# Kernel optimization log

Hardware: AMD Instinct MI355X
Metric: run time of the kernel (lower is better)

The kernel has to match this reference:

```python
import jax, jax.numpy as jnp
import numpy as np

HEADS = 8
DIM_HEAD = 64
SCALE = DIM_HEAD ** -0.5

def setup_inputs() -> dict:
    key = jax.random.key(0)
    ks = jax.random.split(key, 6)
    b, n, m, qd, cd = 4, 2048, 2048, 256, 256
    inner = HEADS * DIM_HEAD
    return {
        "x": jax.random.normal(ks[0], (b, n, qd), jnp.float32),
        "context": jax.random.normal(ks[1], (b, m, cd), jnp.float32),
        "Wq": jax.random.normal(ks[2], (inner, qd), jnp.float32) * 0.02,
        "bq": jnp.zeros((inner,), jnp.float32),
        "Wkv": jax.random.normal(ks[3], (2 * inner, cd), jnp.float32) * 0.02,
        "bkv": jnp.zeros((2 * inner,), jnp.float32),
        "Wo": jax.random.normal(ks[4], (qd, inner), jnp.float32) * 0.02,
        "bo": jnp.zeros((qd,), jnp.float32),
    }

def reference(x, context, Wq, bq, Wkv, bkv, Wo, bo):
    b, n, _ = x.shape
    m = context.shape[1]
    inner = HEADS * DIM_HEAD
    # 1x1 conv projections == pointwise linear
    q = jnp.einsum('bnd,ed->bne', x, Wq) + bq            # [b, n, inner]
    kv = jnp.einsum('bmd,ed->bme', context, Wkv) + bkv    # [b, m, 2*inner]
    k, v = kv[..., :inner], kv[..., inner:]
    q = q.reshape(b, n, HEADS, DIM_HEAD).transpose(0, 2, 1, 3)  # [b,h,n,d]
    k = k.reshape(b, m, HEADS, DIM_HEAD).transpose(0, 2, 1, 3)
    v = v.reshape(b, m, HEADS, DIM_HEAD).transpose(0, 2, 1, 3)
    sim = jnp.einsum('bhid,bhjd->bhij', q, k) * SCALE     # [b,h,n,m]
    attn = jax.nn.softmax(sim, axis=-1)
    out = jnp.einsum('bhij,bhjd->bhid', attn, v)          # [b,h,n,d]
    out = out.transpose(0, 2, 1, 3).reshape(b, n, inner)  # [b,n,inner]
    return jnp.einsum('bne,oe->bno', out, Wo) + bo        # [b,n,query_dim]
```

## Files before the change

kernel.cpp:

```cpp
#include <hip/hip_runtime.h>
#include <hip/hip_bf16.h>

#define NB 4
#define SEQ 2048
#define NHEADS 8
#define ROWS (NB * SEQ)

typedef __attribute__((ext_vector_type(8))) short bf16x8;
typedef __attribute__((ext_vector_type(4))) short bf16x4;
typedef __attribute__((ext_vector_type(4))) float f32x4;
typedef __attribute__((ext_vector_type(16))) float f32x16;

__device__ inline short f2bf(float x) {
    union { float f; unsigned u; } v; v.f = x;
    unsigned r = v.u + 0x7FFF + ((v.u >> 16) & 1);
    return (short)(r >> 16);
}

__device__ inline unsigned pack2bf(float a, float b) {
    __hip_bfloat162 h = __float22bfloat162_rn(make_float2(a, b));
    unsigned u; __builtin_memcpy(&u, &h, 4);
    return u;
}

__device__ inline unsigned comb2(unsigned w1, unsigned w2, float inv) {
    union { unsigned v; float f; } a, b, c, d;
    a.v = w1 << 16;          b.v = w2 << 16;
    c.v = w1 & 0xffff0000u;  d.v = w2 & 0xffff0000u;
    return pack2bf((a.f + b.f) * inv, (c.f + d.f) * inv);
}

__global__ __launch_bounds__(256) void cvt_all(
    const float* __restrict__ x, const float* __restrict__ ctx,
    const float* __restrict__ wq, const float* __restrict__ wkv,
    const float* __restrict__ wo,
    short* __restrict__ xb, short* __restrict__ cb, short* __restrict__ wqb,
    short* __restrict__ wkvb, short* __restrict__ wob)
{
    const int i = blockIdx.x * 256 + threadIdx.x;
    const float* src; short* dst; int off;
    if (i < 524288)       { src = x;   dst = xb;   off = i; }
    else if (i < 1048576) { src = ctx; dst = cb;   off = i - 524288; }
    else if (i < 1081344) { src = wq;  dst = wqb;  off = i - 1048576; }
    else if (i < 1146880) { src = wkv; dst = wkvb; off = i - 1081344; }
    else                  { src = wo;  dst = wob;  off = i - 1146880; }
    const float4 v = ((const float4*)src)[off];
    uint2 o2;
    o2.x = pack2bf(v.x, v.y);
    o2.y = pack2bf(v.z, v.w);
    *(uint2*)(dst + (size_t)off * 4) = o2;
}

__global__ __launch_bounds__(256, 3) void proj2(
    const short* __restrict__ xb, const short* __restrict__ wqb,
    const float* __restrict__ bq,
    const short* __restrict__ cb, const short* __restrict__ wkvb,
    const float* __restrict__ bkv,
    short* __restrict__ q2b, short* __restrict__ kv2b, float qscale)
{
    __shared__ short As[128 * 64];
    __shared__ short Ws[128 * 64];
    const int tid = threadIdx.x;
    const int bid = blockIdx.x;
    const int w = tid >> 6, lane = tid & 63, low = lane & 15, quad = lane >> 4;
    const int wm = w >> 1, wn = w & 1;
    const int K = 256;

    const short* A; const short* W; const float* bias;
    short* outp; int Ccols; float scale; int rM0, c0;
    if (bid < 512) {
        A = cb; W = wkvb; bias = bkv; outp = kv2b; Ccols = 1024; scale = 1.0f;
        c0 = (bid & 7) * 128; rM0 = (bid >> 3) * 128;
    } else {
        const int u = bid - 512;
        A = xb; W = wqb; bias = bq; outp = q2b; Ccols = 512; scale = qscale;
        c0 = (u & 3) * 128; rM0 = (u >> 2) * 128;
    }

    const int srow = tid >> 3, sj = tid & 7;

    f32x4 acc[4][4];
#pragma unroll
    for (int mt = 0; mt < 4; ++mt)
#pragma unroll
        for (int nt = 0; nt < 4; ++nt) acc[mt][nt] = (f32x4){0.f, 0.f, 0.f, 0.f};

    bf16x8 pab[4], pwb[4];
#pragma unroll
    for (int c = 0; c < 4; ++c) {
        const int row = c * 32 + srow;
        pab[c] = *(const bf16x8*)(A + (size_t)(rM0 + row) * K + sj * 8);
        pwb[c] = *(const bf16x8*)(W + (size_t)(c0 + row) * K + sj * 8);
    }

    int k0 = 0;
    for (;;) {
        __syncthreads();
#pragma unroll
        for (int c = 0; c < 4; ++c) {
            const int row = c * 32 + srow;
            const int pc = sj ^ (row & 7);
            *(bf16x8*)(&As[row * 64 + pc * 8]) = pab[c];
            *(bf16x8*)(&Ws[row * 64 + pc * 8]) = pwb[c];
        }
        __syncthreads();
        const int kn = k0 + 64;
        if (kn < K) {
#pragma unroll
            for (int c = 0; c < 4; ++c) {
                const int row = c * 32 + srow;
                pab[c] = *(const bf16x8*)(A + (size_t)(rM0 + row) * K + kn + sj * 8);
                pwb[c] = *(const bf16x8*)(W + (size_t)(c0 + row) * K + kn + sj * 8);
            }
        }
#pragma unroll
        for (int kh = 0; kh < 2; ++kh) {
            bf16x8 af[4], bfv[4];
#pragma unroll
            for (int t = 0; t < 4; ++t) {
                const int ra = wm * 64 + t * 16 + low;
                af[t] = *(const bf16x8*)(&As[ra * 64 + ((kh * 4 + quad) ^ (ra & 7)) * 8]);
                const int rb = wn * 64 + t * 16 + low;
                bfv[t] = *(const bf16x8*)(&Ws[rb * 64 + ((kh * 4 + quad) ^ (rb & 7)) * 8]);
            }
#pragma unroll
            for (int mt = 0; mt < 4; ++mt)
#pragma unroll
                for (int nt = 0; nt < 4; ++nt)
                    acc[mt][nt] = __builtin_amdgcn_mfma_f32_16x16x32_bf16(af[mt], bfv[nt], acc[mt][nt], 0, 0, 0);
        }
        k0 = kn;
        if (k0 >= K) break;
    }

#pragma unroll
    for (int nt = 0; nt < 4; ++nt) {
        const int col = c0 + wn * 64 + nt * 16 + low;
        const float bv = bias[col];
#pragma unroll
        for (int mt = 0; mt < 4; ++mt) {
            const size_t rbase = (size_t)(rM0 + wm * 64 + mt * 16 + quad * 4);
#pragma unroll
            for (int r = 0; r < 4; ++r)
                outp[(rbase + r) * Ccols + col] = f2bf((acc[mt][nt][r] + bv) * scale);
        }
    }
}

__global__ __launch_bounds__(256, 2) void gemm64_ocomb(
    const short* __restrict__ num, const float* __restrict__ lbuf,
    const short* __restrict__ W, const float* __restrict__ bias,
    float* __restrict__ out)
{
    const int K = 512, Ccols = 256;
    const size_t NHALF = (size_t)ROWS * 512;
    const int R8 = ROWS * 8;
    __shared__ short As[2][64 * 64];
    __shared__ short Ws[2][64 * 64];
    const int tid = threadIdx.x;
    const int w = tid >> 6, lane = tid & 63, low = lane & 15, quad = lane >> 4;
    const int wm = w >> 1, wn = w & 1;

    const int d = blockIdx.x;
    const int c8 = d & 7, j = d >> 3;
    const int xcol = j & 3;
    const int y = ((j >> 2) << 3) + c8;
    const int r0 = y * 64, c0 = xcol * 64;

    const int srow = tid >> 2;
    const int sc = (tid & 3) * 2;

    f32x4 acc[2][2];
#pragma unroll
    for (int mt = 0; mt < 2; ++mt)
#pragma unroll
        for (int nt = 0; nt < 2; ++nt) acc[mt][nt] = (f32x4){0.f, 0.f, 0.f, 0.f};

    uint4 pa1[2], pa2[2];
    float pinv;
    bf16x8 pwb[2];

    auto loadA = [&](int k0) {
        const int hh = k0 >> 6;
        const int row = r0 + srow;
        pinv = lbuf[row * 8 + hh] + lbuf[R8 + row * 8 + hh];
        const short* p1 = num + (size_t)row * 512 + k0 + sc * 8;
        pa1[0] = ((const uint4*)p1)[0];
        pa1[1] = ((const uint4*)p1)[1];
        const short* p2 = p1 + NHALF;
        pa2[0] = ((const uint4*)p2)[0];
        pa2[1] = ((const uint4*)p2)[1];
    };
    auto loadW = [&](int k0) {
        const short* p = W + (size_t)(c0 + srow) * K + k0 + sc * 8;
        pwb[0] = ((const bf16x8*)p)[0];
        pwb[1] = ((const bf16x8*)p)[1];
    };
    auto stage = [&](int bi) {
        const float inv = 1.f / pinv;
#pragma unroll
        for (int c = 0; c < 2; ++c) {
            const int pc = (sc + c) ^ (srow & 7);
            union { unsigned u[4]; bf16x8 v; } r;
            r.u[0] = comb2(pa1[c].x, pa2[c].x, inv);
            r.u[1] = comb2(pa1[c].y, pa2[c].y, inv);
            r.u[2] = comb2(pa1[c].z, pa2[c].z, inv);
            r.u[3] = comb2(pa1[c].w, pa2[c].w, inv);
            *(bf16x8*)(&As[bi][srow * 64 + pc * 8]) = r.v;
            *(bf16x8*)(&Ws[bi][srow * 64 + pc * 8]) = pwb[c];
        }
    };

    loadA(0); loadW(0);
    stage(0);
    __syncthreads();

    const int NT = K / 64;
    for (int t = 0; t < NT; ++t) {
        if (t + 1 < NT) { loadA((t + 1) * 64); loadW((t + 1) * 64); }

        const short* Ac = &As[t & 1][0];
        const short* Wc = &Ws[t & 1][0];
#pragma unroll
        for (int kh = 0; kh < 2; ++kh) {
            bf16x8 af[2], bfv[2];
#pragma unroll
            for (int tt = 0; tt < 2; ++tt) {
                const int ra = wm * 32 + tt * 16 + low;
                af[tt] = *(const bf16x8*)(&Ac[ra * 64 + ((kh * 4 + quad) ^ (ra & 7)) * 8]);
                const int rb = wn * 32 + tt * 16 + low;
                bfv[tt] = *(const bf16x8*)(&Wc[rb * 64 + ((kh * 4 + quad) ^ (rb & 7)) * 8]);
            }
#pragma unroll
            for (int mt = 0; mt < 2; ++mt)
#pragma unroll
                for (int nt = 0; nt < 2; ++nt)
                    acc[mt][nt] = __builtin_amdgcn_mfma_f32_16x16x32_bf16(af[mt], bfv[nt], acc[mt][nt], 0, 0, 0);
        }

        if (t + 1 < NT) stage((t + 1) & 1);
        __syncthreads();
    }

#pragma unroll
    for (int nt = 0; nt < 2; ++nt) {
        const int col = c0 + wn * 32 + nt * 16 + low;
        const float bv = bias[col];
#pragma unroll
        for (int mt = 0; mt < 2; ++mt) {
            const size_t rbase = (size_t)(r0 + wm * 32 + mt * 16 + quad * 4);
#pragma unroll
            for (int r = 0; r < 4; ++r)
                out[(rbase + r) * Ccols + col] = acc[mt][nt][r] + bv;
        }
    }
}

#define KST 72
#define VST 72

__global__ __launch_bounds__(256, 4) void attn_mfma(
    const short* __restrict__ q2,
    const short* __restrict__ kv2,
    short* __restrict__ numb,
    float* __restrict__ lbuf)
{
    __shared__ short Ks[64 * KST];
    __shared__ short Vt[64 * VST];

    const int tid = threadIdx.x;
    const int w = tid >> 6;
    const int lane = tid & 63;
    const int l31 = lane & 31;
    const int h2 = lane >> 5;

    const int flat = blockIdx.x;
    const int h = flat & 7;
    const int rest = flat >> 3;
    const int half = rest & 1;
    const int rest2 = rest >> 1;
    const int qtile = rest2 & 15;
    const int b = rest2 >> 4;
    const int iq0 = qtile * 128;
    const int jt0 = half * 16;

    bf16x8 qr[4];
#pragma unroll
    for (int st = 0; st < 4; ++st)
        qr[st] = *(const bf16x8*)(q2 + (size_t)(b * SEQ + iq0 + w * 32 + l31) * 512
                                  + h * 64 + st * 16 + h2 * 8);

    const short* kbase = kv2 + (size_t)(b * SEQ) * 1024 + h * 64;
    const short* vbase = kbase + 512;

    float lsum = 0.f;
    f32x16 oacc[2];
#pragma unroll
    for (int dg = 0; dg < 2; ++dg)
#pragma unroll
        for (int r = 0; r < 16; ++r) oacc[dg][r] = 0.f;

    const int krow = tid >> 2;
    const int kc = (tid & 3) * 16;
    const int vk4 = (tid & 15) * 4;
    const int vd4 = (tid >> 4) * 4;

    bf16x8 pk0, pk1;
    bf16x4 pv0, pv1, pv2, pv3;
    {
        const short* ksrc = kbase + (size_t)(jt0 * 64 + krow) * 1024 + kc;
        pk0 = *(const bf16x8*)(ksrc);
        pk1 = *(const bf16x8*)(ksrc + 8);
        const short* vs = vbase + (size_t)(jt0 * 64 + vk4) * 1024 + vd4;
        pv0 = *(const bf16x4*)(vs);
        pv1 = *(const bf16x4*)(vs + 1024);
        pv2 = *(const bf16x4*)(vs + 2048);
        pv3 = *(const bf16x4*)(vs + 3072);
    }

    for (int jt = jt0; jt < jt0 + 16; ++jt) {
        __syncthreads();
        *(bf16x8*)(&Ks[krow * KST + kc]) = pk0;
        *(bf16x8*)(&Ks[krow * KST + kc + 8]) = pk1;
        {
            bf16x4 c0_, c1_, c2_, c3_;
            c0_[0] = pv0[0]; c0_[1] = pv1[0]; c0_[2] = pv2[0]; c0_[3] = pv3[0];
            c1_[0] = pv0[1]; c1_[1] = pv1[1]; c1_[2] = pv2[1]; c1_[3] = pv3[1];
            c2_[0] = pv0[2]; c2_[1] = pv1[2]; c2_[2] = pv2[2]; c2_[3] = pv3[2];
            c3_[0] = pv0[3]; c3_[1] = pv1[3]; c3_[2] = pv2[3]; c3_[3] = pv3[3];
            *(bf16x4*)(&Vt[(vd4 + 0) * VST + vk4]) = c0_;
            *(bf16x4*)(&Vt[(vd4 + 1) * VST + vk4]) = c1_;
            *(bf16x4*)(&Vt[(vd4 + 2) * VST + vk4]) = c2_;
            *(bf16x4*)(&Vt[(vd4 + 3) * VST + vk4]) = c3_;
        }
        __syncthreads();

        if (jt + 1 < jt0 + 16) {
            const short* ksrc = kbase + (size_t)((jt + 1) * 64 + krow) * 1024 + kc;
            pk0 = *(const bf16x8*)(ksrc);
            pk1 = *(const bf16x8*)(ksrc + 8);
            const short* vs = vbase + (size_t)((jt + 1) * 64 + vk4) * 1024 + vd4;
            pv0 = *(const bf16x4*)(vs);
            pv1 = *(const bf16x4*)(vs + 1024);
            pv2 = *(const bf16x4*)(vs + 2048);
            pv3 = *(const bf16x4*)(vs + 3072);
        }

        bf16x8 pfrag[4];
#pragma unroll
        for (int kg = 0; kg < 2; ++kg) {
            f32x16 s;
#pragma unroll
            for (int r = 0; r < 16; ++r) s[r] = 0.f;
#pragma unroll
            for (int st = 0; st < 4; ++st) {
                const bf16x8 kf = *(const bf16x8*)(&Ks[(kg * 32 + l31) * KST + st * 16 + h2 * 8]);
                s = __builtin_amdgcn_mfma_f32_32x32x16_bf16(kf, qr[st], s, 0, 0, 0);
            }
            unsigned wv[8];
#pragma unroll
            for (int g = 0; g < 4; ++g) {
                const float p0 = __builtin_amdgcn_exp2f(s[4 * g + 0]);
                const float p1 = __builtin_amdgcn_exp2f(s[4 * g + 1]);
                const float p2 = __builtin_amdgcn_exp2f(s[4 * g + 2]);
                const float p3 = __builtin_amdgcn_exp2f(s[4 * g + 3]);
                lsum += (p0 + p1) + (p2 + p3);
                wv[2 * g]     = pack2bf(p0, p1);
                wv[2 * g + 1] = pack2bf(p2, p3);
            }
#pragma unroll
            for (int q = 0; q < 2; ++q) {
                unsigned a0 = wv[4 * q + 0], b0 = wv[4 * q + 2];
                unsigned a1 = wv[4 * q + 1], b1 = wv[4 * q + 3];
                asm volatile("v_permlane32_swap_b32 %0, %1" : "+v"(a0), "+v"(b0));
                asm volatile("v_permlane32_swap_b32 %0, %1" : "+v"(a1), "+v"(b1));
                union { unsigned u[4]; bf16x8 v; } f;
                f.u[0] = a0; f.u[1] = a1; f.u[2] = b0; f.u[3] = b1;
                pfrag[kg * 2 + q] = f.v;
            }
        }

#pragma unroll
        for (int st = 0; st < 4; ++st) {
            const bf16x8 pf = pfrag[st];
#pragma unroll
            for (int dg = 0; dg < 2; ++dg) {
                const bf16x8 vf = *(const bf16x8*)(&Vt[(dg * 32 + l31) * VST + st * 16 + h2 * 8]);
                oacc[dg] = __builtin_amdgcn_mfma_f32_32x32x16_bf16(pf, vf, oacc[dg], 0, 0, 0);
            }
        }
    }

    lsum += __shfl_xor(lsum, 32);
    short* nb = numb + (size_t)half * ROWS * 512;
    float* lb = lbuf + (size_t)half * ROWS * 8;
    if (lane < 32)
        lb[(size_t)(b * SEQ + iq0 + w * 32 + l31) * 8 + h] = lsum;
#pragma unroll
    for (int dg = 0; dg < 2; ++dg)
#pragma unroll
        for (int r = 0; r < 16; ++r) {
            const int qrow = w * 32 + (r & 3) + 8 * (r >> 2) + 4 * h2;
            nb[(size_t)(b * SEQ + iq0 + qrow) * 512 + h * 64 + dg * 32 + l31] =
                f2bf(oacc[dg][r]);
        }
}

extern "C" void kernel_launch(void* const* d_in, const int* in_sizes, int n_in,
                              void* d_out, int out_size, void* d_ws, size_t ws_size,
                              hipStream_t stream) {
    const float* x   = (const float*)d_in[0];
    const float* ctx = (const float*)d_in[1];
    const float* Wq  = (const float*)d_in[2];
    const float* bq  = (const float*)d_in[3];
    const float* Wkv = (const float*)d_in[4];
    const float* bkv = (const float*)d_in[5];
    const float* Wo  = (const float*)d_in[6];
    const float* bo  = (const float*)d_in[7];
    float* out = (float*)d_out;

    short* xb   = (short*)d_ws;
    short* cb   = xb + (size_t)ROWS * 256;
    short* wqb  = cb + (size_t)ROWS * 256;
    short* wkvb = wqb + 131072;
    short* wob  = wkvb + 262144;
    short* q2b  = wob + 131072;
    short* kv2b = q2b + (size_t)ROWS * 512;
    short* numb = kv2b + (size_t)ROWS * 1024;
    float* lbuf = (float*)(numb + (size_t)2 * ROWS * 512);

    const float qscale = 0.125f * 1.44269504088896f;

    cvt_all<<<4608, 256, 0, stream>>>(x, ctx, Wq, Wkv, Wo,
                                      xb, cb, wqb, wkvb, wob);
    proj2<<<768, 256, 0, stream>>>(xb, wqb, bq, cb, wkvb, bkv,
                                   q2b, kv2b, qscale);
    attn_mfma<<<NB * NHEADS * (SEQ / 128) * 2, 256, 0, stream>>>(
        q2b, kv2b, numb, lbuf);
    gemm64_ocomb<<<512, 256, 0, stream>>>(numb, lbuf, wob, bo, out);
}
```

Measured before the change: 152.5 us.

## Move split-K attention combine into the block via LDS reduction

Previously each attention block handled 128 queries over half the keys and wrote partial bf16 numerators plus row sums, which the output GEMM then combined and normalized. Now each block handles 64 queries. The four warps split into two query groups and two key halves, double-buffered in LDS, and the halves are reduced through shared memory so a normalized output is written directly. This removes the double-sized partial buffer traffic and the combine arithmetic in the output GEMM. In exchange it uses twice the LDS, cuts the occupancy hint from 4 to 2, and adds an in-block reduction step.

```diff
diff --git a/kernel.cpp b/kernel.cpp
--- a/kernel.cpp
+++ b/kernel.cpp
@@ -21,13 +21,6 @@
     __hip_bfloat162 h = __float22bfloat162_rn(make_float2(a, b));
     unsigned u; __builtin_memcpy(&u, &h, 4);
     return u;
-}
-
-__device__ inline unsigned comb2(unsigned w1, unsigned w2, float inv) {
-    union { unsigned v; float f; } a, b, c, d;
-    a.v = w1 << 16;          b.v = w2 << 16;
-    c.v = w1 & 0xffff0000u;  d.v = w2 & 0xffff0000u;
-    return pack2bf((a.f + b.f) * inv, (c.f + d.f) * inv);
 }
 
 __global__ __launch_bounds__(256) void cvt_all(
@@ -147,14 +140,11 @@
     }
 }
 
-__global__ __launch_bounds__(256, 2) void gemm64_ocomb(
-    const short* __restrict__ num, const float* __restrict__ lbuf,
-    const short* __restrict__ W, const float* __restrict__ bias,
-    float* __restrict__ out)
+__global__ __launch_bounds__(256, 2) void gemm64_o(
+    const short* __restrict__ Ab, const short* __restrict__ W,
+    const float* __restrict__ bias, float* __restrict__ out)
 {
     const int K = 512, Ccols = 256;
-    const size_t NHALF = (size_t)ROWS * 512;
-    const int R8 = ROWS * 8;
     __shared__ short As[2][64 * 64];
     __shared__ short Ws[2][64 * 64];
     const int tid = threadIdx.x;
@@ -176,20 +166,12 @@
 #pragma unroll
         for (int nt = 0; nt < 2; ++nt) acc[mt][nt] = (f32x4){0.f, 0.f, 0.f, 0.f};
 
-    uint4 pa1[2], pa2[2];
-    float pinv;
-    bf16x8 pwb[2];
+    bf16x8 pa[2], pwb[2];
 
     auto loadA = [&](int k0) {
-        const int hh = k0 >> 6;
-        const int row = r0 + srow;
-        pinv = lbuf[row * 8 + hh] + lbuf[R8 + row * 8 + hh];
-        const short* p1 = num + (size_t)row * 512 + k0 + sc * 8;
-        pa1[0] = ((const uint4*)p1)[0];
-        pa1[1] = ((const uint4*)p1)[1];
-        const short* p2 = p1 + NHALF;
-        pa2[0] = ((const uint4*)p2)[0];
-        pa2[1] = ((const uint4*)p2)[1];
+        const short* p = Ab + (size_t)(r0 + srow) * 512 + k0 + sc * 8;
+        pa[0] = ((const bf16x8*)p)[0];
+        pa[1] = ((const bf16x8*)p)[1];
     };
     auto loadW = [&](int k0) {
         const short* p = W + (size_t)(c0 + srow) * K + k0 + sc * 8;
@@ -197,16 +179,10 @@
         pwb[1] = ((const bf16x8*)p)[1];
     };
     auto stage = [&](int bi) {
-        const float inv = 1.f / pinv;
 #pragma unroll
         for (int c = 0; c < 2; ++c) {
             const int pc = (sc + c) ^ (srow & 7);
-            union { unsigned u[4]; bf16x8 v; } r;
-            r.u[0] = comb2(pa1[c].x, pa2[c].x, inv);
-            r.u[1] = comb2(pa1[c].y, pa2[c].y, inv);
-            r.u[2] = comb2(pa1[c].z, pa2[c].z, inv);
-            r.u[3] = comb2(pa1[c].w, pa2[c].w, inv);
-            *(bf16x8*)(&As[bi][srow * 64 + pc * 8]) = r.v;
+            *(bf16x8*)(&As[bi][srow * 64 + pc * 8]) = pa[c];
             *(bf16x8*)(&Ws[bi][srow * 64 + pc * 8]) = pwb[c];
         }
     };
@@ -259,35 +235,33 @@
 #define KST 72
 #define VST 72
 
-__global__ __launch_bounds__(256, 4) void attn_mfma(
+__global__ __launch_bounds__(256, 2) void attn_mfma(
     const short* __restrict__ q2,
     const short* __restrict__ kv2,
-    short* __restrict__ numb,
-    float* __restrict__ lbuf)
+    short* __restrict__ ob)
 {
-    __shared__ short Ks[64 * KST];
-    __shared__ short Vt[64 * VST];
+    __shared__ short Ks[2][64 * KST];
+    __shared__ short Vt[2][64 * VST];
 
     const int tid = threadIdx.x;
     const int w = tid >> 6;
     const int lane = tid & 63;
     const int l31 = lane & 31;
     const int h2 = lane >> 5;
+    const int wq = w & 1;
+    const int wh = w >> 1;
 
     const int flat = blockIdx.x;
     const int h = flat & 7;
     const int rest = flat >> 3;
-    const int half = rest & 1;
-    const int rest2 = rest >> 1;
-    const int qtile = rest2 & 15;
-    const int b = rest2 >> 4;
-    const int iq0 = qtile * 128;
-    const int jt0 = half * 16;
+    const int qtile = rest & 31;
+    const int b = rest >> 5;
+    const int iq0 = qtile * 64;
 
     bf16x8 qr[4];
 #pragma unroll
     for (int st = 0; st < 4; ++st)
-        qr[st] = *(const bf16x8*)(q2 + (size_t)(b * SEQ + iq0 + w * 32 + l31) * 512
+        qr[st] = *(const bf16x8*)(q2 + (size_t)(b * SEQ + iq0 + wq * 32 + l31) * 512
                                   + h * 64 + st * 16 + h2 * 8);
 
     const short* kbase = kv2 + (size_t)(b * SEQ) * 1024 + h * 64;
@@ -305,47 +279,56 @@
     const int vk4 = (tid & 15) * 4;
     const int vd4 = (tid >> 4) * 4;
 
-    bf16x8 pk0, pk1;
-    bf16x4 pv0, pv1, pv2, pv3;
-    {
-        const short* ksrc = kbase + (size_t)(jt0 * 64 + krow) * 1024 + kc;
-        pk0 = *(const bf16x8*)(ksrc);
-        pk1 = *(const bf16x8*)(ksrc + 8);
-        const short* vs = vbase + (size_t)(jt0 * 64 + vk4) * 1024 + vd4;
-        pv0 = *(const bf16x4*)(vs);
-        pv1 = *(const bf16x4*)(vs + 1024);
-        pv2 = *(const bf16x4*)(vs + 2048);
-        pv3 = *(const bf16x4*)(vs + 3072);
-    }
-
-    for (int jt = jt0; jt < jt0 + 16; ++jt) {
+    bf16x8 pk0[2], pk1[2];
+    bf16x4 pv0[2], pv1[2], pv2[2], pv3[2];
+#pragma unroll
+    for (int t = 0; t < 2; ++t) {
+        const int kt = t * 16;
+        const short* ksrc = kbase + (size_t)(kt * 64 + krow) * 1024 + kc;
+        pk0[t] = *(const bf16x8*)(ksrc);
+        pk1[t] = *(const bf16x8*)(ksrc + 8);
+        const short* vs = vbase + (size_t)(kt * 64 + vk4) * 1024 + vd4;
+        pv0[t] = *(const bf16x4*)(vs);
+        pv1[t] = *(const bf16x4*)(vs + 1024);
+        pv2[t] = *(const bf16x4*)(vs + 2048);
+        pv3[t] = *(const bf16x4*)(vs + 3072);
+    }
+
+    for (int jt = 0; jt < 16; ++jt) {
         __syncthreads();
-        *(bf16x8*)(&Ks[krow * KST + kc]) = pk0;
-        *(bf16x8*)(&Ks[krow * KST + kc + 8]) = pk1;
-        {
+#pragma unroll
+        for (int t = 0; t < 2; ++t) {
+            *(bf16x8*)(&Ks[t][krow * KST + kc]) = pk0[t];
+            *(bf16x8*)(&Ks[t][krow * KST + kc + 8]) = pk1[t];
             bf16x4 c0_, c1_, c2_, c3_;
-            c0_[0] = pv0[0]; c0_[1] = pv1[0]; c0_[2] = pv2[0]; c0_[3] = pv3[0];
-            c1_[0] = pv0[1]; c1_[1] = pv1[1]; c1_[2] = pv2[1]; c1_[3] = pv3[1];
-            c2_[0] = pv0[2]; c2_[1] = pv1[2]; c2_[2] = pv2[2]; c2_[3] = pv3[2];
-            c3_[0] = pv0[3]; c3_[1] = pv1[3]; c3_[2] = pv2[3]; c3_[3] = pv3[3];
-            *(bf16x4*)(&Vt[(vd4 + 0) * VST + vk4]) = c0_;
-            *(bf16x4*)(&Vt[(vd4 + 1) * VST + vk4]) = c1_;
-            *(bf16x4*)(&Vt[(vd4 + 2) * VST + vk4]) = c2_;
-            *(bf16x4*)(&Vt[(vd4 + 3) * VST + vk4]) = c3_;
+            c0_[0] = pv0[t][0]; c0_[1] = pv1[t][0]; c0_[2] = pv2[t][0]; c0_[3] = pv3[t][0];
+            c1_[0] = pv0[t][1]; c1_[1] = pv1[t][1]; c1_[2] = pv2[t][1]; c1_[3] = pv3[t][1];
+            c2_[0] = pv0[t][2]; c2_[1] = pv1[t][2]; c2_[2] = pv2[t][2]; c2_[3] = pv3[t][2];
+            c3_[0] = pv0[t][3]; c3_[1] = pv1[t][3]; c3_[2] = pv2[t][3]; c3_[3] = pv3[t][3];
+            *(bf16x4*)(&Vt[t][(vd4 + 0) * VST + vk4]) = c0_;
+            *(bf16x4*)(&Vt[t][(vd4 + 1) * VST + vk4]) = c1_;
+            *(bf16x4*)(&Vt[t][(vd4 + 2) * VST + vk4]) = c2_;
+            *(bf16x4*)(&Vt[t][(vd4 + 3) * VST + vk4]) = c3_;
         }
         __syncthreads();
 
-        if (jt + 1 < jt0 + 16) {
-            const short* ksrc = kbase + (size_t)((jt + 1) * 64 + krow) * 1024 + kc;
-            pk0 = *(const bf16x8*)(ksrc);
-            pk1 = *(const bf16x8*)(ksrc + 8);
-            const short* vs = vbase + (size_t)((jt + 1) * 64 + vk4) * 1024 + vd4;
-            pv0 = *(const bf16x4*)(vs);
-            pv1 = *(const bf16x4*)(vs + 1024);
-            pv2 = *(const bf16x4*)(vs + 2048);
-            pv3 = *(const bf16x4*)(vs + 3072);
-        }
-
+        if (jt + 1 < 16) {
+#pragma unroll
+            for (int t = 0; t < 2; ++t) {
+                const int kt = t * 16 + jt + 1;
+                const short* ksrc = kbase + (size_t)(kt * 64 + krow) * 1024 + kc;
+                pk0[t] = *(const bf16x8*)(ksrc);
+                pk1[t] = *(const bf16x8*)(ksrc + 8);
+                const short* vs = vbase + (size_t)(kt * 64 + vk4) * 1024 + vd4;
+                pv0[t] = *(const bf16x4*)(vs);
+                pv1[t] = *(const bf16x4*)(vs + 1024);
+                pv2[t] = *(const bf16x4*)(vs + 2048);
+                pv3[t] = *(const bf16x4*)(vs + 3072);
+            }
+        }
+
+        const short* Kc = &Ks[wh][0];
+        const short* Vc = &Vt[wh][0];
         bf16x8 pfrag[4];
 #pragma unroll
         for (int kg = 0; kg < 2; ++kg) {
@@ -354,7 +337,7 @@
             for (int r = 0; r < 16; ++r) s[r] = 0.f;
 #pragma unroll
             for (int st = 0; st < 4; ++st) {
-                const bf16x8 kf = *(const bf16x8*)(&Ks[(kg * 32 + l31) * KST + st * 16 + h2 * 8]);
+                const bf16x8 kf = *(const bf16x8*)(&Kc[(kg * 32 + l31) * KST + st * 16 + h2 * 8]);
                 s = __builtin_amdgcn_mfma_f32_32x32x16_bf16(kf, qr[st], s, 0, 0, 0);
             }
             unsigned wv[8];
@@ -385,25 +368,39 @@
             const bf16x8 pf = pfrag[st];
 #pragma unroll
             for (int dg = 0; dg < 2; ++dg) {
-                const bf16x8 vf = *(const bf16x8*)(&Vt[(dg * 32 + l31) * VST + st * 16 + h2 * 8]);
+                const bf16x8 vf = *(const bf16x8*)(&Vc[(dg * 32 + l31) * VST + st * 16 + h2 * 8]);
                 oacc[dg] = __builtin_amdgcn_mfma_f32_32x32x16_bf16(pf, vf, oacc[dg], 0, 0, 0);
             }
         }
     }
 
     lsum += __shfl_xor(lsum, 32);
-    short* nb = numb + (size_t)half * ROWS * 512;
-    float* lb = lbuf + (size_t)half * ROWS * 8;
-    if (lane < 32)
-        lb[(size_t)(b * SEQ + iq0 + w * 32 + l31) * 8 + h] = lsum;
-#pragma unroll
-    for (int dg = 0; dg < 2; ++dg)
+    __syncthreads();
+    float* fbuf = (float*)(&Ks[0][0]);
+    float* lred = (float*)(&Vt[0][0]);
+    if (wh == 1) {
+#pragma unroll
+        for (int dg = 0; dg < 2; ++dg)
+#pragma unroll
+            for (int r = 0; r < 16; ++r)
+                fbuf[(wq * 64 + lane) * 32 + dg * 16 + r] = oacc[dg][r];
+        if (lane < 32) lred[wq * 32 + l31] = lsum;
+    }
+    __syncthreads();
+    if (wh == 0) {
+        if (lane < 32) lred[wq * 32 + l31] += lsum;
+        short* nb = ob + (size_t)(b * SEQ + iq0 + wq * 32) * 512 + h * 64;
 #pragma unroll
         for (int r = 0; r < 16; ++r) {
-            const int qrow = w * 32 + (r & 3) + 8 * (r >> 2) + 4 * h2;
-            nb[(size_t)(b * SEQ + iq0 + qrow) * 512 + h * 64 + dg * 32 + l31] =
-                f2bf(oacc[dg][r]);
-        }
+            const int qrow = (r & 3) + 8 * (r >> 2) + 4 * h2;
+            const float inv = 1.0f / lred[wq * 32 + qrow];
+#pragma unroll
+            for (int dg = 0; dg < 2; ++dg) {
+                const float o = oacc[dg][r] + fbuf[(wq * 64 + lane) * 32 + dg * 16 + r];
+                nb[(size_t)qrow * 512 + dg * 32 + l31] = f2bf(o * inv);
+            }
+        }
+    }
 }
 
 extern "C" void kernel_launch(void* const* d_in, const int* in_sizes, int n_in,
@@ -426,8 +423,7 @@
     short* wob  = wkvb + 262144;
     short* q2b  = wob + 131072;
     short* kv2b = q2b + (size_t)ROWS * 512;
-    short* numb = kv2b + (size_t)ROWS * 1024;
-    float* lbuf = (float*)(numb + (size_t)2 * ROWS * 512);
+    short* obuf = kv2b + (size_t)ROWS * 1024;
 
     const float qscale = 0.125f * 1.44269504088896f;
 
@@ -435,7 +431,7 @@
                                       xb, cb, wqb, wkvb, wob);
     proj2<<<768, 256, 0, stream>>>(xb, wqb, bq, cb, wkvb, bkv,
                                    q2b, kv2b, qscale);
-    attn_mfma<<<NB * NHEADS * (SEQ / 128) * 2, 256, 0, stream>>>(
-        q2b, kv2b, numb, lbuf);
-    gemm64_ocomb<<<512, 256, 0, stream>>>(numb, lbuf, wob, bo, out);
-}
+    attn_mfma<<<NB * NHEADS * (SEQ / 64), 256, 0, stream>>>(
+        q2b, kv2b, obuf);
+    gemm64_o<<<512, 256, 0, stream>>>(obuf, wob, bo, out);
+}
```

New measurement: 182.4 us. +19.6%, slower.
